# Kernel tuning notes

Measured on AMD Instinct MI355X. Metric: run time of the kernel, lower is better.

The kernel has to match this reference:

```python
import jax, jax.numpy as jnp
import numpy as np

T, N, E, IN, H, H2, H3, B, AF = 12, 50000, 800000, 12, 128, 64, 32, 4096, 10
BN_EPS = 1e-5


def _gin_mlp(h, w1, b1, g, be, rm, rv, w2, b2):
    # Linear -> ReLU -> BatchNorm1d (eval: running stats) -> Dropout(eval=id) -> Linear -> ReLU
    h = jax.nn.relu(h @ w1.T + b1)
    h = (h - rm) * (g * jax.lax.rsqrt(rv + BN_EPS)) + be
    return jax.nn.relu(h @ w2.T + b2)


def _gin_conv(x, edge_src, edge_dst, mlp_params):
    # GINConv with eps=0: MLP(x + sum_{j in N(i)} x_j), scatter-add over edges
    agg = jax.ops.segment_sum(x[edge_src], edge_dst, num_segments=x.shape[0])
    return _gin_mlp(x + agg, *mlp_params)


def _gru(xs, wih, whh, bih, bhh):
    # torch.nn.GRU, 1 layer, h0 = zeros. xs: [T, N, H_in]
    h0 = jnp.zeros((xs.shape[1], whh.shape[1]), xs.dtype)

    def step(h, x):
        gi = x @ wih.T + bih
        gh = h @ whh.T + bhh
        ir, iz, inn = jnp.split(gi, 3, axis=-1)
        hr, hz, hn = jnp.split(gh, 3, axis=-1)
        r = jax.nn.sigmoid(ir + hr)
        z = jax.nn.sigmoid(iz + hz)
        n = jnp.tanh(inn + r * hn)
        h_new = (1.0 - z) * n + z * h
        return h_new, h_new

    h_last, ys = jax.lax.scan(step, h0, xs)
    return ys, h_last


def _forward(floats, edge_src, edge_dst, target_idx):
    (x_seq, apart_feature,
     c1_w1, c1_b1, c1_g, c1_be, c1_rm, c1_rv, c1_w2, c1_b2,
     c2_w1, c2_b1, c2_g, c2_be, c2_rm, c2_rv, c2_w2, c2_b2,
     gru_wih, gru_whh, gru_bih, gru_bhh,
     fc1_w, fc1_b, fc2_w, fc2_b, fc3_w, fc3_b) = floats

    c1 = (c1_w1, c1_b1, c1_g, c1_be, c1_rm, c1_rv, c1_w2, c1_b2)
    c2 = (c2_w1, c2_b1, c2_g, c2_be, c2_rm, c2_rv, c2_w2, c2_b2)

    # conv1 per time slot (lax.map keeps the E x H gather intermediate per-step)
    # extra torch.relu after conv1 is a no-op since the MLP ends in ReLU
    emb = jax.lax.map(lambda xt: _gin_conv(xt, edge_src, edge_dst, c1), x_seq)
    seq, _ = _gru(emb, gru_wih, gru_whh, gru_bih, gru_bhh)
    emb2 = jax.lax.map(lambda xt: _gin_conv(xt, edge_src, edge_dst, c2), seq)
    _, h_last = _gru(emb2, gru_wih, gru_whh, gru_bih, gru_bhh)  # same GRU weights reused

    feat = jnp.concatenate([h_last[target_idx], apart_feature], axis=1)
    h = jax.nn.leaky_relu(feat @ fc1_w.T + fc1_b, negative_slope=0.1)
    h = jax.nn.leaky_relu(h @ fc2_w.T + fc2_b, negative_slope=0.05)
    return h @ fc3_w.T + fc3_b  # [B, 1]


def setup_inputs() -> dict:
    key = jax.random.key(0)
    ks = jax.random.split(key, 24)
    f32 = jnp.float32
    w = lambda i, shape, fan: jax.random.normal(ks[i], shape, f32) * (1.0 / np.sqrt(fan))
    return {
        "x_seq": jax.random.normal(ks[0], (T, N, IN), f32),
        "apart_feature": jax.random.normal(ks[1], (B, AF), f32),
        "edge_src": jax.random.randint(ks[2], (E,), 0, N, jnp.int32),
        "edge_dst": jax.random.randint(ks[3], (E,), 0, N, jnp.int32),
        "target_idx": jax.random.randint(ks[4], (B,), 0, N, jnp.int32),
        # conv1 MLP
        "c1_w1": w(5, (H, IN), IN), "c1_b1": jnp.zeros((H,), f32),
        "c1_g": jnp.ones((H,), f32), "c1_be": jnp.zeros((H,), f32),
        "c1_rm": jnp.zeros((H,), f32), "c1_rv": jnp.ones((H,), f32),
        "c1_w2": w(6, (H, H), H), "c1_b2": jnp.zeros((H,), f32),
        # conv2 MLP
        "c2_w1": w(7, (H, H), H), "c2_b1": jnp.zeros((H,), f32),
        "c2_g": jnp.ones((H,), f32), "c2_be": jnp.zeros((H,), f32),
        "c2_rm": jnp.zeros((H,), f32), "c2_rv": jnp.ones((H,), f32),
        "c2_w2": w(8, (H, H), H), "c2_b2": jnp.zeros((H,), f32),
        # shared GRU
        "gru_wih": w(9, (3 * H, H), H), "gru_whh": w(10, (3 * H, H), H),
        "gru_bih": jnp.zeros((3 * H,), f32), "gru_bhh": jnp.zeros((3 * H,), f32),
        # head
        "fc1_w": w(11, (H2, H + AF), H + AF), "fc1_b": jnp.zeros((H2,), f32),
        "fc2_w": w(12, (H3, H2), H2), "fc2_b": jnp.zeros((H3,), f32),
        "fc3_w": w(13, (1, H3), H3), "fc3_b": jnp.zeros((1,), f32),
    }


def reference(x_seq, apart_feature,
              c1_w1, c1_b1, c1_g, c1_be, c1_rm, c1_rv, c1_w2, c1_b2,
              c2_w1, c2_b1, c2_g, c2_be, c2_rm, c2_rv, c2_w2, c2_b2,
              gru_wih, gru_whh, gru_bih, gru_bhh,
              fc1_w, fc1_b, fc2_w, fc2_b, fc3_w, fc3_b,
              edge_src, edge_dst, target_idx):
    floats = (x_seq, apart_feature,
              c1_w1, c1_b1, c1_g, c1_be, c1_rm, c1_rv, c1_w2, c1_b2,
              c2_w1, c2_b1, c2_g, c2_be, c2_rm, c2_rv, c2_w2, c2_b2,
              gru_wih, gru_whh, gru_bih, gru_bhh,
              fc1_w, fc1_b, fc2_w, fc2_b, fc3_w, fc3_b)
    return _forward(floats, edge_src, edge_dst, target_idx)
```

## Files before the change

kernel.cpp:

```cpp
#include <hip/hip_runtime.h>

#define T_STEPS 12
#define NN      50000
#define EE      800000
#define IN_F    12
#define HID     128
#define G3      384
#define BB      4096
#define AF_     10
#define BN_EPS  1e-5f
#define LPAD    136

typedef unsigned short ushort_t;
typedef __attribute__((ext_vector_type(8))) short bf16x8;
typedef __attribute__((ext_vector_type(4))) float f32x4;

#define MFMA(a, b, c) __builtin_amdgcn_mfma_f32_16x16x32_bf16((a), (b), (c), 0, 0, 0)

__device__ inline float b2f(ushort_t u) { return __uint_as_float(((unsigned)u) << 16); }
__device__ inline ushort_t f2b(float f) {
    unsigned u = __float_as_uint(f);
    return (ushort_t)((u + 0x7fffu + ((u >> 16) & 1u)) >> 16);
}
__device__ inline float sigm(float x) { return 1.f / (1.f + expf(-x)); }

#define ALIGN_UP(x) (((x) + 255) & ~(size_t)255)
#define SZ_DEG    ALIGN_UP((size_t)NN * 4)
#define SZ_RP     ALIGN_UP((size_t)(NN + 1) * 4)
#define SZ_CUR    ALIGN_UP((size_t)NN * 4)
#define SZ_COL    ALIGN_UP((size_t)EE * 4)
#define SZ_XIN12  ALIGN_UP((size_t)NN * IN_F * 4)
#define SZ_NHB    ALIGN_UP((size_t)NN * HID * 2)
#define SZ_W128   ALIGN_UP((size_t)HID * HID * 2)
#define SZ_WGRU   ALIGN_UP((size_t)G3 * HID * 2)
#define WS_NEED   (SZ_DEG + SZ_RP + SZ_CUR + SZ_COL + SZ_XIN12 + 3 * SZ_NHB + 3 * SZ_W128 + 2 * SZ_WGRU)

__device__ __align__(256) char g_static_pool[WS_NEED];

__global__ void zero_out_kernel(float* out, int n) {
    int i = blockIdx.x * blockDim.x + threadIdx.x;
    if (i < n) out[i] = 0.f;
}

__global__ void cvt5_kernel(const float* s0, ushort_t* d0, int n0,
                            const float* s1, ushort_t* d1, int n1,
                            const float* s2, ushort_t* d2, int n2,
                            const float* s3, ushort_t* d3, int n3,
                            const float* s4, ushort_t* d4, int n4) {
    int i = blockIdx.x * blockDim.x + threadIdx.x;
    if (i < n0) d0[i] = f2b(s0[i]);
    i -= n0;
    if (i >= 0 && i < n1) d1[i] = f2b(s1[i]);
    i -= n1;
    if (i >= 0 && i < n2) d2[i] = f2b(s2[i]);
    i -= n2;
    if (i >= 0 && i < n3) d3[i] = f2b(s3[i]);
    i -= n3;
    if (i >= 0 && i < n4) d4[i] = f2b(s4[i]);
}

__global__ void init_kernel(int* deg, ushort_t* h1, ushort_t* h2) {
    int i = blockIdx.x * blockDim.x + threadIdx.x;
    if (i < NN) deg[i] = 0;
    if (i < NN * HID) { h1[i] = 0; h2[i] = 0; }
}

__global__ void hist_kernel(const int* __restrict__ dst, int* __restrict__ deg, int E) {
    int e = blockIdx.x * blockDim.x + threadIdx.x;
    if (e < E) {
        unsigned d = (unsigned)dst[e];
        if (d < NN) atomicAdd(&deg[d], 1);
    }
}

__global__ __launch_bounds__(1024) void scan_kernel(const int* __restrict__ deg,
                                                    int* __restrict__ row_ptr,
                                                    int* __restrict__ cursor, int n) {
    __shared__ int wsum[16];
    __shared__ int carry_s;
    int tid = threadIdx.x;
    int wid = tid >> 6, lane = tid & 63;
    if (tid == 0) { carry_s = 0; row_ptr[0] = 0; }
    __syncthreads();
    for (int base = 0; base < n; base += 1024) {
        int i = base + tid;
        int v = (i < n) ? deg[i] : 0;
        int x = v;
#pragma unroll
        for (int off = 1; off < 64; off <<= 1) {
            int t = __shfl_up(x, (unsigned)off);
            if (lane >= off) x += t;
        }
        if (lane == 63) wsum[wid] = x;
        __syncthreads();
        if (tid == 0) {
            int a = 0;
#pragma unroll
            for (int w = 0; w < 16; ++w) { int t = wsum[w]; wsum[w] = a; a += t; }
        }
        __syncthreads();
        int incl = carry_s + wsum[wid] + x;
        if (i < n) {
            row_ptr[i + 1] = incl;
            cursor[i] = incl - v;
        }
        __syncthreads();
        if (tid == 1023) carry_s = incl;
        __syncthreads();
    }
}

__global__ void scatter_kernel(const int* __restrict__ src, const int* __restrict__ dst,
                               int* __restrict__ cursor, int* __restrict__ col, int E) {
    int e = blockIdx.x * blockDim.x + threadIdx.x;
    if (e < E) {
        unsigned d = (unsigned)dst[e];
        if (d < NN) {
            int pos = atomicAdd(&cursor[d], 1);
            if ((unsigned)pos < (unsigned)EE) col[pos] = src[e];
        }
    }
}

__global__ void agg12_kernel(const float* __restrict__ x, const int* __restrict__ rp,
                             const int* __restrict__ col, float* __restrict__ out, int E) {
    int g = blockIdx.x * blockDim.x + threadIdx.x;
    if (g >= NN * IN_F) return;
    int i = g / IN_F;
    int f = g - i * IN_F;
    float s = x[g];
    int e0 = rp[i], e1 = rp[i + 1];
    if (e1 > E) e1 = E;
    for (int e = e0; e < e1; ++e) {
        unsigned c = (unsigned)col[e];
        if (c < NN) s += x[c * IN_F + f];
    }
    out[g] = s;
}

__device__ __forceinline__ void gru_phase(const ushort_t (*xl)[LPAD], ushort_t* __restrict__ h,
                                          const ushort_t* __restrict__ wih, const ushort_t* __restrict__ whh,
                                          const float* __restrict__ bih, const float* __restrict__ bhh,
                                          int r0, int li, int ks, int wave) {
    int j0 = wave * 16;
    int ra0 = min(r0 + li, NN - 1);
    int ra1 = min(r0 + 16 + li, NN - 1);
    const ushort_t* ph0 = h + (size_t)ra0 * HID + ks * 8;
    const ushort_t* ph1 = h + (size_t)ra1 * HID + ks * 8;
    const ushort_t* pwr = wih + (size_t)(j0 + li) * HID + ks * 8;
    const ushort_t* pwz = wih + (size_t)(HID + j0 + li) * HID + ks * 8;
    const ushort_t* pwn = wih + (size_t)(2 * HID + j0 + li) * HID + ks * 8;
    const ushort_t* pvr = whh + (size_t)(j0 + li) * HID + ks * 8;
    const ushort_t* pvz = whh + (size_t)(HID + j0 + li) * HID + ks * 8;
    const ushort_t* pvn = whh + (size_t)(2 * HID + j0 + li) * HID + ks * 8;
    f32x4 ir0 = {0,0,0,0}, iz0 = {0,0,0,0}, in0 = {0,0,0,0};
    f32x4 hr0 = {0,0,0,0}, hz0 = {0,0,0,0}, hn0 = {0,0,0,0};
    f32x4 ir1 = {0,0,0,0}, iz1 = {0,0,0,0}, in1 = {0,0,0,0};
    f32x4 hr1 = {0,0,0,0}, hz1 = {0,0,0,0}, hn1 = {0,0,0,0};
#pragma unroll
    for (int k0 = 0; k0 < HID; k0 += 32) {
        bf16x8 ax0 = *(const bf16x8*)&xl[li][ks * 8 + k0];
        bf16x8 ax1 = *(const bf16x8*)&xl[li + 16][ks * 8 + k0];
        bf16x8 ah0 = *(const bf16x8*)(ph0 + k0);
        bf16x8 ah1 = *(const bf16x8*)(ph1 + k0);
        bf16x8 br = *(const bf16x8*)(pwr + k0);
        bf16x8 bz = *(const bf16x8*)(pwz + k0);
        bf16x8 bn = *(const bf16x8*)(pwn + k0);
        bf16x8 cr = *(const bf16x8*)(pvr + k0);
        bf16x8 cz = *(const bf16x8*)(pvz + k0);
        bf16x8 cn = *(const bf16x8*)(pvn + k0);
        ir0 = MFMA(ax0, br, ir0); ir1 = MFMA(ax1, br, ir1);
        iz0 = MFMA(ax0, bz, iz0); iz1 = MFMA(ax1, bz, iz1);
        in0 = MFMA(ax0, bn, in0); in1 = MFMA(ax1, bn, in1);
        hr0 = MFMA(ah0, cr, hr0); hr1 = MFMA(ah1, cr, hr1);
        hz0 = MFMA(ah0, cz, hz0); hz1 = MFMA(ah1, cz, hz1);
        hn0 = MFMA(ah0, cn, hn0); hn1 = MFMA(ah1, cn, hn1);
    }
    int jc = j0 + li;
    float bi_r = bih[jc], bi_z = bih[HID + jc], bi_n = bih[2 * HID + jc];
    float bh_r = bhh[jc], bh_z = bhh[HID + jc], bh_n = bhh[2 * HID + jc];
    float holdA[4], holdB[4];
#pragma unroll
    for (int q = 0; q < 4; ++q) {
        int rowA = min(r0 + ks * 4 + q, NN - 1);
        int rowB = min(r0 + 16 + ks * 4 + q, NN - 1);
        holdA[q] = b2f(h[(size_t)rowA * HID + jc]);
        holdB[q] = b2f(h[(size_t)rowB * HID + jc]);
    }
    __syncthreads();
#pragma unroll
    for (int q = 0; q < 4; ++q) {
        int rowA = r0 + ks * 4 + q;
        int rowB = rowA + 16;
        {
            float rg = sigm(ir0[q] + bi_r + hr0[q] + bh_r);
            float zg = sigm(iz0[q] + bi_z + hz0[q] + bh_z);
            float ng = tanhf(in0[q] + bi_n + rg * (hn0[q] + bh_n));
            float hv = (1.f - zg) * ng + zg * holdA[q];
            if (rowA < NN) h[(size_t)rowA * HID + jc] = f2b(hv);
        }
        {
            float rg = sigm(ir1[q] + bi_r + hr1[q] + bh_r);
            float zg = sigm(iz1[q] + bi_z + hz1[q] + bh_z);
            float ng = tanhf(in1[q] + bi_n + rg * (hn1[q] + bh_n));
            float hv = (1.f - zg) * ng + zg * holdB[q];
            if (rowB < NN) h[(size_t)rowB * HID + jc] = f2b(hv);
        }
    }
}

__global__ __launch_bounds__(512) void mega1_kernel(const float* __restrict__ xin12,
                                                    ushort_t* __restrict__ h,
                                                    const float* __restrict__ W1, const float* __restrict__ b1,
                                                    const float* __restrict__ gg, const float* __restrict__ be,
                                                    const float* __restrict__ rm, const float* __restrict__ rv,
                                                    const ushort_t* __restrict__ w2b, const float* __restrict__ b2,
                                                    const ushort_t* __restrict__ wih, const ushort_t* __restrict__ whh,
                                                    const float* __restrict__ bih, const float* __restrict__ bhh) {
    __shared__ float xs[32][IN_F];
    __shared__ ushort_t l1[32][LPAD];
    __shared__ ushort_t l2[32][LPAD];
    int tid = threadIdx.x;
    int wave = tid >> 6, lane = tid & 63;
    int li = lane & 15, ks = lane >> 4;
    int r0 = blockIdx.x * 32;
    if (tid < 32 * IN_F) {
        int r = tid / IN_F, f = tid - r * IN_F;
        int row = r0 + r;
        xs[r][f] = (row < NN) ? xin12[(size_t)row * IN_F + f] : 0.f;
    }
    __syncthreads();
    {
        int j = tid & 127, rb = tid >> 7;
        float sc = gg[j] * rsqrtf(rv[j] + BN_EPS);
        float sh = be[j] - rm[j] * sc;
        float bj = b1[j];
        float wreg[IN_F];
#pragma unroll
        for (int k = 0; k < IN_F; ++k) wreg[k] = W1[j * IN_F + k];
#pragma unroll
        for (int q = 0; q < 8; ++q) {
            int r = rb + q * 4;
            float s = bj;
#pragma unroll
            for (int k = 0; k < IN_F; ++k) s += xs[r][k] * wreg[k];
            s = fmaxf(s, 0.f);
            l1[r][j] = f2b(s * sc + sh);
        }
    }
    __syncthreads();
    {
        int j0 = wave * 16;
        const ushort_t* pw = w2b + (size_t)(j0 + li) * HID + ks * 8;
        f32x4 acc0 = {0,0,0,0}, acc1 = {0,0,0,0};
#pragma unroll
        for (int k0 = 0; k0 < HID; k0 += 32) {
            bf16x8 w = *(const bf16x8*)(pw + k0);
            bf16x8 a0 = *(const bf16x8*)&l1[li][ks * 8 + k0];
            bf16x8 a1 = *(const bf16x8*)&l1[li + 16][ks * 8 + k0];
            acc0 = MFMA(a0, w, acc0);
            acc1 = MFMA(a1, w, acc1);
        }
        float bj = b2[j0 + li];
#pragma unroll
        for (int q = 0; q < 4; ++q) {
            l2[ks * 4 + q][j0 + li] = f2b(fmaxf(acc0[q] + bj, 0.f));
            l2[16 + ks * 4 + q][j0 + li] = f2b(fmaxf(acc1[q] + bj, 0.f));
        }
    }
    __syncthreads();
    gru_phase(l2, h, wih, whh, bih, bhh, r0, li, ks, wave);
}

__global__ __launch_bounds__(512) void mega2_kernel(const ushort_t* __restrict__ xin2,
                                                    ushort_t* __restrict__ h,
                                                    const ushort_t* __restrict__ w1b, const float* __restrict__ b1,
                                                    const float* __restrict__ gg, const float* __restrict__ be,
                                                    const float* __restrict__ rm, const float* __restrict__ rv,
                                                    const ushort_t* __restrict__ w2b, const float* __restrict__ b2,
                                                    const ushort_t* __restrict__ wih, const ushort_t* __restrict__ whh,
                                                    const float* __restrict__ bih, const float* __restrict__ bhh) {
    __shared__ ushort_t l1[32][LPAD];
    __shared__ ushort_t l2[32][LPAD];
    int tid = threadIdx.x;
    int wave = tid >> 6, lane = tid & 63;
    int li = lane & 15, ks = lane >> 4;
    int r0 = blockIdx.x * 32;
    {
        int j0 = wave * 16;
        int ra0 = min(r0 + li, NN - 1);
        int ra1 = min(r0 + 16 + li, NN - 1);
        const ushort_t* pa0 = xin2 + (size_t)ra0 * HID + ks * 8;
        const ushort_t* pa1 = xin2 + (size_t)ra1 * HID + ks * 8;
        const ushort_t* pw = w1b + (size_t)(j0 + li) * HID + ks * 8;
        f32x4 acc0 = {0,0,0,0}, acc1 = {0,0,0,0};
#pragma unroll
        for (int k0 = 0; k0 < HID; k0 += 32) {
            bf16x8 w = *(const bf16x8*)(pw + k0);
            bf16x8 a0 = *(const bf16x8*)(pa0 + k0);
            bf16x8 a1 = *(const bf16x8*)(pa1 + k0);
            acc0 = MFMA(a0, w, acc0);
            acc1 = MFMA(a1, w, acc1);
        }
        int jc = j0 + li;
        float sc = gg[jc] * rsqrtf(rv[jc] + BN_EPS);
        float sh = be[jc] - rm[jc] * sc;
        float bj = b1[jc];
#pragma unroll
        for (int q = 0; q < 4; ++q) {
            l1[ks * 4 + q][jc] = f2b(fmaxf(acc0[q] + bj, 0.f) * sc + sh);
            l1[16 + ks * 4 + q][jc] = f2b(fmaxf(acc1[q] + bj, 0.f) * sc + sh);
        }
    }
    __syncthreads();
    {
        int j0 = wave * 16;
        const ushort_t* pw = w2b + (size_t)(j0 + li) * HID + ks * 8;
        f32x4 acc0 = {0,0,0,0}, acc1 = {0,0,0,0};
#pragma unroll
        for (int k0 = 0; k0 < HID; k0 += 32) {
            bf16x8 w = *(const bf16x8*)(pw + k0);
            bf16x8 a0 = *(const bf16x8*)&l1[li][ks * 8 + k0];
            bf16x8 a1 = *(const bf16x8*)&l1[li + 16][ks * 8 + k0];
            acc0 = MFMA(a0, w, acc0);
            acc1 = MFMA(a1, w, acc1);
        }
        float bj = b2[j0 + li];
#pragma unroll
        for (int q = 0; q < 4; ++q) {
            l2[ks * 4 + q][j0 + li] = f2b(fmaxf(acc0[q] + bj, 0.f));
            l2[16 + ks * 4 + q][j0 + li] = f2b(fmaxf(acc1[q] + bj, 0.f));
        }
    }
    __syncthreads();
    gru_phase(l2, h, wih, whh, bih, bhh, r0, li, ks, wave);
}

__global__ __launch_bounds__(256) void agg128b_kernel(const ushort_t* __restrict__ x,
                                                      const int* __restrict__ rp,
                                                      const int* __restrict__ col,
                                                      ushort_t* __restrict__ out, int E) {
    int node = (blockIdx.x * 256 + threadIdx.x) >> 6;
    int lane = threadIdx.x & 63;
    if (node >= NN) return;
    unsigned v = *(const unsigned*)(x + (size_t)node * HID + lane * 2);
    float s0 = b2f((ushort_t)(v & 0xffff));
    float s1 = b2f((ushort_t)(v >> 16));
    int e0 = rp[node], e1 = rp[node + 1];
    if (e1 > E) e1 = E;
    int e = e0;
    for (; e + 3 < e1; e += 4) {
        unsigned c0 = (unsigned)col[e], c1 = (unsigned)col[e + 1];
        unsigned c2 = (unsigned)col[e + 2], c3 = (unsigned)col[e + 3];
        c0 = (c0 < NN) ? c0 : 0; c1 = (c1 < NN) ? c1 : 0;
        c2 = (c2 < NN) ? c2 : 0; c3 = (c3 < NN) ? c3 : 0;
        unsigned u0 = *(const unsigned*)(x + (size_t)c0 * HID + lane * 2);
        unsigned u1 = *(const unsigned*)(x + (size_t)c1 * HID + lane * 2);
        unsigned u2 = *(const unsigned*)(x + (size_t)c2 * HID + lane * 2);
        unsigned u3 = *(const unsigned*)(x + (size_t)c3 * HID + lane * 2);
        s0 += b2f((ushort_t)(u0 & 0xffff)) + b2f((ushort_t)(u1 & 0xffff))
            + b2f((ushort_t)(u2 & 0xffff)) + b2f((ushort_t)(u3 & 0xffff));
        s1 += b2f((ushort_t)(u0 >> 16)) + b2f((ushort_t)(u1 >> 16))
            + b2f((ushort_t)(u2 >> 16)) + b2f((ushort_t)(u3 >> 16));
    }
    for (; e < e1; ++e) {
        unsigned c = (unsigned)col[e];
        if (c < NN) {
            unsigned u = *(const unsigned*)(x + (size_t)c * HID + lane * 2);
            s0 += b2f((ushort_t)(u & 0xffff));
            s1 += b2f((ushort_t)(u >> 16));
        }
    }
    unsigned o = (unsigned)f2b(s0) | ((unsigned)f2b(s1) << 16);
    *(unsigned*)(out + (size_t)node * HID + lane * 2) = o;
}

__global__ __launch_bounds__(64) void head_kernel(const ushort_t* __restrict__ h2, const int* __restrict__ tidx,
                                                  const float* __restrict__ apart,
                                                  const float* __restrict__ w1, const float* __restrict__ b1,
                                                  const float* __restrict__ w2, const float* __restrict__ b2,
                                                  const float* __restrict__ w3, const float* __restrict__ b3,
                                                  float* __restrict__ out) {
    __shared__ float feat[HID + AF_];
    __shared__ float o1[64];
    __shared__ float o2[32];
    int b = blockIdx.x;
    int t = threadIdx.x;
    unsigned node = (unsigned)tidx[b];
    if (node >= NN) node = 0;
    for (int k = t; k < HID; k += 64) feat[k] = b2f(h2[(size_t)node * HID + k]);
    if (t < AF_) feat[HID + t] = apart[(size_t)b * AF_ + t];
    __syncthreads();
    {
        float s = b1[t];
        for (int k = 0; k < HID + AF_; ++k) s += feat[k] * w1[t * (HID + AF_) + k];
        o1[t] = (s > 0.f) ? s : 0.1f * s;
    }
    __syncthreads();
    if (t < 32) {
        float s = b2[t];
        for (int k = 0; k < 64; ++k) s += o1[k] * w2[t * 64 + k];
        o2[t] = (s > 0.f) ? s : 0.05f * s;
    }
    __syncthreads();
    if (t == 0) {
        float s = b3[0];
        for (int k = 0; k < 32; ++k) s += o2[k] * w3[k];
        out[b] = s;
    }
}

extern "C" void kernel_launch(void* const* d_in, const int* in_sizes, int n_in,
                              void* d_out, int out_size, void* d_ws, size_t ws_size,
                              hipStream_t stream) {
    int ie_src = -1, ie_dst = -1, ie_tidx = -1, iw0 = -1;
    bool ok = false;
    if (n_in >= 31 && in_sizes[0] == T_STEPS * NN * IN_F && in_sizes[1] == BB * AF_) {
        if (in_sizes[2] > 100000 && in_sizes[3] == in_sizes[2] && in_sizes[4] == BB &&
            in_sizes[5] == HID * IN_F && in_sizes[11] == HID * HID &&
            in_sizes[21] == G3 * HID && in_sizes[22] == G3 * HID &&
            in_sizes[25] == 64 * (HID + AF_)) {
            ie_src = 2; ie_dst = 3; ie_tidx = 4; iw0 = 5; ok = true;
        } else if (in_sizes[2] == HID * IN_F && in_sizes[8] == HID * HID &&
                   in_sizes[18] == G3 * HID && in_sizes[19] == G3 * HID &&
                   in_sizes[22] == 64 * (HID + AF_) &&
                   in_sizes[28] > 100000 && in_sizes[29] == in_sizes[28] && in_sizes[30] == BB) {
            iw0 = 2; ie_src = 28; ie_dst = 29; ie_tidx = 30; ok = true;
        }
    }
    if (!ok) {
        zero_out_kernel<<<(out_size + 255) / 256, 256, 0, stream>>>((float*)d_out, out_size);
        return;
    }

    const float* x_seq  = (const float*)d_in[0];
    const float* apart  = (const float*)d_in[1];
    const int*   e_src  = (const int*)d_in[ie_src];
    const int*   e_dst  = (const int*)d_in[ie_dst];
    const int*   t_idx  = (const int*)d_in[ie_tidx];
    const float* c1_w1 = (const float*)d_in[iw0 + 0];
    const float* c1_b1 = (const float*)d_in[iw0 + 1];
    const float* c1_g  = (const float*)d_in[iw0 + 2];
    const float* c1_be = (const float*)d_in[iw0 + 3];
    const float* c1_rm = (const float*)d_in[iw0 + 4];
    const float* c1_rv = (const float*)d_in[iw0 + 5];
    const float* c1_w2 = (const float*)d_in[iw0 + 6];
    const float* c1_b2 = (const float*)d_in[iw0 + 7];
    const float* c2_w1 = (const float*)d_in[iw0 + 8];
    const float* c2_b1 = (const float*)d_in[iw0 + 9];
    const float* c2_g  = (const float*)d_in[iw0 + 10];
    const float* c2_be = (const float*)d_in[iw0 + 11];
    const float* c2_rm = (const float*)d_in[iw0 + 12];
    const float* c2_rv = (const float*)d_in[iw0 + 13];
    const float* c2_w2 = (const float*)d_in[iw0 + 14];
    const float* c2_b2 = (const float*)d_in[iw0 + 15];
    const float* g_wih = (const float*)d_in[iw0 + 16];
    const float* g_whh = (const float*)d_in[iw0 + 17];
    const float* g_bih = (const float*)d_in[iw0 + 18];
    const float* g_bhh = (const float*)d_in[iw0 + 19];
    const float* f1_w  = (const float*)d_in[iw0 + 20];
    const float* f1_b  = (const float*)d_in[iw0 + 21];
    const float* f2_w  = (const float*)d_in[iw0 + 22];
    const float* f2_b  = (const float*)d_in[iw0 + 23];
    const float* f3_w  = (const float*)d_in[iw0 + 24];
    const float* f3_b  = (const float*)d_in[iw0 + 25];

    int E = in_sizes[ie_src];
    if (E > EE) E = EE;

    char* base;
    if (ws_size >= WS_NEED) {
        base = (char*)d_ws;
    } else {
        void* sp = nullptr;
        hipGetSymbolAddress(&sp, HIP_SYMBOL(g_static_pool));
        if (sp == nullptr) {
            zero_out_kernel<<<(out_size + 255) / 256, 256, 0, stream>>>((float*)d_out, out_size);
            return;
        }
        base = (char*)sp;
    }
    size_t off = 0;
    auto nxt = [&](size_t bytes) { char* p = base + off; off += bytes; return p; };
    int*      deg     = (int*)nxt(SZ_DEG);
    int*      row_ptr = (int*)nxt(SZ_RP);
    int*      cursor  = (int*)nxt(SZ_CUR);
    int*      col     = (int*)nxt(SZ_COL);
    float*    xin12   = (float*)nxt(SZ_XIN12);
    ushort_t* xin2    = (ushort_t*)nxt(SZ_NHB);
    ushort_t* h1      = (ushort_t*)nxt(SZ_NHB);
    ushort_t* h2      = (ushort_t*)nxt(SZ_NHB);
    ushort_t* wb_c1w2 = (ushort_t*)nxt(SZ_W128);
    ushort_t* wb_c2w1 = (ushort_t*)nxt(SZ_W128);
    ushort_t* wb_c2w2 = (ushort_t*)nxt(SZ_W128);
    ushort_t* wb_wih  = (ushort_t*)nxt(SZ_WGRU);
    ushort_t* wb_whh  = (ushort_t*)nxt(SZ_WGRU);

    const int NW = 3 * HID * HID + 2 * G3 * HID;
    cvt5_kernel<<<(NW + 255) / 256, 256, 0, stream>>>(c1_w2, wb_c1w2, HID * HID,
                                                      c2_w1, wb_c2w1, HID * HID,
                                                      c2_w2, wb_c2w2, HID * HID,
                                                      g_wih, wb_wih, G3 * HID,
                                                      g_whh, wb_whh, G3 * HID);

    init_kernel<<<(NN * HID + 255) / 256, 256, 0, stream>>>(deg, h1, h2);

    hist_kernel<<<(E + 255) / 256, 256, 0, stream>>>(e_dst, deg, E);
    scan_kernel<<<1, 1024, 0, stream>>>(deg, row_ptr, cursor, NN);
    scatter_kernel<<<(E + 255) / 256, 256, 0, stream>>>(e_src, e_dst, cursor, col, E);

    const int mgrid = (NN + 31) / 32;

    for (int t = 0; t < T_STEPS; ++t) {
        const float* xt = x_seq + (size_t)t * NN * IN_F;
        agg12_kernel<<<(NN * IN_F + 255) / 256, 256, 0, stream>>>(xt, row_ptr, col, xin12, E);
        mega1_kernel<<<mgrid, 512, 0, stream>>>(xin12, h1,
                                                c1_w1, c1_b1, c1_g, c1_be, c1_rm, c1_rv,
                                                wb_c1w2, c1_b2,
                                                wb_wih, wb_whh, g_bih, g_bhh);
        agg128b_kernel<<<(NN * 64 + 255) / 256, 256, 0, stream>>>(h1, row_ptr, col, xin2, E);
        mega2_kernel<<<mgrid, 512, 0, stream>>>(xin2, h2,
                                                wb_c2w1, c2_b1, c2_g, c2_be, c2_rm, c2_rv,
                                                wb_c2w2, c2_b2,
                                                wb_wih, wb_whh, g_bih, g_bhh);
    }

    head_kernel<<<BB, 64, 0, stream>>>(h2, t_idx, apart, f1_w, f1_b, f2_w, f2_b, f3_w, f3_b, (float*)d_out);
}
```

Before: 2.696 ms.

## Batch conv1 over all timesteps, fuse aggregation into conv2 kernel, enlarge tiles

Conv1 no longer depends on the recurrence, so it now runs for all 12 timesteps in one launch that also does the 12-feature neighbour sum inline. It writes a T×N×H bf16 embedding buffer that a separate per-step GRU kernel reads. The 128-wide neighbour aggregation moves inside mega2, which removes the agg128b launch and its intermediate round trip. Row tiles grow from 32 to 64 and sigmoid/tanh switch to exp2/rcp intrinsics. In exchange it needs about 150MB of extra workspace and does more work per block, which may lower occupancy.

```diff
diff --git a/kernel.cpp b/kernel.cpp
--- a/kernel.cpp
+++ b/kernel.cpp
@@ -16,24 +16,34 @@
 typedef __attribute__((ext_vector_type(4))) float f32x4;
 
 #define MFMA(a, b, c) __builtin_amdgcn_mfma_f32_16x16x32_bf16((a), (b), (c), 0, 0, 0)
+#define L2E 1.4426950408889634f
 
 __device__ inline float b2f(ushort_t u) { return __uint_as_float(((unsigned)u) << 16); }
+__device__ inline float b2f_lo(unsigned u) { return __uint_as_float(u << 16); }
+__device__ inline float b2f_hi(unsigned u) { return __uint_as_float(u & 0xffff0000u); }
 __device__ inline ushort_t f2b(float f) {
     unsigned u = __float_as_uint(f);
     return (ushort_t)((u + 0x7fffu + ((u >> 16) & 1u)) >> 16);
 }
-__device__ inline float sigm(float x) { return 1.f / (1.f + expf(-x)); }
+__device__ inline float sigm(float x) {
+    return __builtin_amdgcn_rcpf(1.f + __builtin_amdgcn_exp2f(-x * L2E));
+}
+__device__ inline float ftanh(float x) {
+    float xx = fminf(fmaxf(x, -15.f), 15.f);
+    float t = __builtin_amdgcn_exp2f(2.f * L2E * xx);
+    return (t - 1.f) * __builtin_amdgcn_rcpf(t + 1.f);
+}
 
 #define ALIGN_UP(x) (((x) + 255) & ~(size_t)255)
 #define SZ_DEG    ALIGN_UP((size_t)NN * 4)
 #define SZ_RP     ALIGN_UP((size_t)(NN + 1) * 4)
 #define SZ_CUR    ALIGN_UP((size_t)NN * 4)
 #define SZ_COL    ALIGN_UP((size_t)EE * 4)
-#define SZ_XIN12  ALIGN_UP((size_t)NN * IN_F * 4)
+#define SZ_EMB    ALIGN_UP((size_t)T_STEPS * NN * HID * 2)
 #define SZ_NHB    ALIGN_UP((size_t)NN * HID * 2)
 #define SZ_W128   ALIGN_UP((size_t)HID * HID * 2)
 #define SZ_WGRU   ALIGN_UP((size_t)G3 * HID * 2)
-#define WS_NEED   (SZ_DEG + SZ_RP + SZ_CUR + SZ_COL + SZ_XIN12 + 3 * SZ_NHB + 3 * SZ_W128 + 2 * SZ_WGRU)
+#define WS_NEED   (SZ_DEG + SZ_RP + SZ_CUR + SZ_COL + SZ_EMB + 2 * SZ_NHB + 3 * SZ_W128 + 2 * SZ_WGRU)
 
 __device__ __align__(256) char g_static_pool[WS_NEED];
 
@@ -122,112 +132,35 @@
     }
 }
 
-__global__ void agg12_kernel(const float* __restrict__ x, const int* __restrict__ rp,
-                             const int* __restrict__ col, float* __restrict__ out, int E) {
-    int g = blockIdx.x * blockDim.x + threadIdx.x;
-    if (g >= NN * IN_F) return;
-    int i = g / IN_F;
-    int f = g - i * IN_F;
-    float s = x[g];
-    int e0 = rp[i], e1 = rp[i + 1];
-    if (e1 > E) e1 = E;
-    for (int e = e0; e < e1; ++e) {
-        unsigned c = (unsigned)col[e];
-        if (c < NN) s += x[c * IN_F + f];
-    }
-    out[g] = s;
-}
-
-__device__ __forceinline__ void gru_phase(const ushort_t (*xl)[LPAD], ushort_t* __restrict__ h,
-                                          const ushort_t* __restrict__ wih, const ushort_t* __restrict__ whh,
-                                          const float* __restrict__ bih, const float* __restrict__ bhh,
-                                          int r0, int li, int ks, int wave) {
-    int j0 = wave * 16;
-    int ra0 = min(r0 + li, NN - 1);
-    int ra1 = min(r0 + 16 + li, NN - 1);
-    const ushort_t* ph0 = h + (size_t)ra0 * HID + ks * 8;
-    const ushort_t* ph1 = h + (size_t)ra1 * HID + ks * 8;
-    const ushort_t* pwr = wih + (size_t)(j0 + li) * HID + ks * 8;
-    const ushort_t* pwz = wih + (size_t)(HID + j0 + li) * HID + ks * 8;
-    const ushort_t* pwn = wih + (size_t)(2 * HID + j0 + li) * HID + ks * 8;
-    const ushort_t* pvr = whh + (size_t)(j0 + li) * HID + ks * 8;
-    const ushort_t* pvz = whh + (size_t)(HID + j0 + li) * HID + ks * 8;
-    const ushort_t* pvn = whh + (size_t)(2 * HID + j0 + li) * HID + ks * 8;
-    f32x4 ir0 = {0,0,0,0}, iz0 = {0,0,0,0}, in0 = {0,0,0,0};
-    f32x4 hr0 = {0,0,0,0}, hz0 = {0,0,0,0}, hn0 = {0,0,0,0};
-    f32x4 ir1 = {0,0,0,0}, iz1 = {0,0,0,0}, in1 = {0,0,0,0};
-    f32x4 hr1 = {0,0,0,0}, hz1 = {0,0,0,0}, hn1 = {0,0,0,0};
-#pragma unroll
-    for (int k0 = 0; k0 < HID; k0 += 32) {
-        bf16x8 ax0 = *(const bf16x8*)&xl[li][ks * 8 + k0];
-        bf16x8 ax1 = *(const bf16x8*)&xl[li + 16][ks * 8 + k0];
-        bf16x8 ah0 = *(const bf16x8*)(ph0 + k0);
-        bf16x8 ah1 = *(const bf16x8*)(ph1 + k0);
-        bf16x8 br = *(const bf16x8*)(pwr + k0);
-        bf16x8 bz = *(const bf16x8*)(pwz + k0);
-        bf16x8 bn = *(const bf16x8*)(pwn + k0);
-        bf16x8 cr = *(const bf16x8*)(pvr + k0);
-        bf16x8 cz = *(const bf16x8*)(pvz + k0);
-        bf16x8 cn = *(const bf16x8*)(pvn + k0);
-        ir0 = MFMA(ax0, br, ir0); ir1 = MFMA(ax1, br, ir1);
-        iz0 = MFMA(ax0, bz, iz0); iz1 = MFMA(ax1, bz, iz1);
-        in0 = MFMA(ax0, bn, in0); in1 = MFMA(ax1, bn, in1);
-        hr0 = MFMA(ah0, cr, hr0); hr1 = MFMA(ah1, cr, hr1);
-        hz0 = MFMA(ah0, cz, hz0); hz1 = MFMA(ah1, cz, hz1);
-        hn0 = MFMA(ah0, cn, hn0); hn1 = MFMA(ah1, cn, hn1);
-    }
-    int jc = j0 + li;
-    float bi_r = bih[jc], bi_z = bih[HID + jc], bi_n = bih[2 * HID + jc];
-    float bh_r = bhh[jc], bh_z = bhh[HID + jc], bh_n = bhh[2 * HID + jc];
-    float holdA[4], holdB[4];
-#pragma unroll
-    for (int q = 0; q < 4; ++q) {
-        int rowA = min(r0 + ks * 4 + q, NN - 1);
-        int rowB = min(r0 + 16 + ks * 4 + q, NN - 1);
-        holdA[q] = b2f(h[(size_t)rowA * HID + jc]);
-        holdB[q] = b2f(h[(size_t)rowB * HID + jc]);
-    }
-    __syncthreads();
-#pragma unroll
-    for (int q = 0; q < 4; ++q) {
-        int rowA = r0 + ks * 4 + q;
-        int rowB = rowA + 16;
-        {
-            float rg = sigm(ir0[q] + bi_r + hr0[q] + bh_r);
-            float zg = sigm(iz0[q] + bi_z + hz0[q] + bh_z);
-            float ng = tanhf(in0[q] + bi_n + rg * (hn0[q] + bh_n));
-            float hv = (1.f - zg) * ng + zg * holdA[q];
-            if (rowA < NN) h[(size_t)rowA * HID + jc] = f2b(hv);
-        }
-        {
-            float rg = sigm(ir1[q] + bi_r + hr1[q] + bh_r);
-            float zg = sigm(iz1[q] + bi_z + hz1[q] + bh_z);
-            float ng = tanhf(in1[q] + bi_n + rg * (hn1[q] + bh_n));
-            float hv = (1.f - zg) * ng + zg * holdB[q];
-            if (rowB < NN) h[(size_t)rowB * HID + jc] = f2b(hv);
-        }
-    }
-}
-
-__global__ __launch_bounds__(512) void mega1_kernel(const float* __restrict__ xin12,
-                                                    ushort_t* __restrict__ h,
-                                                    const float* __restrict__ W1, const float* __restrict__ b1,
-                                                    const float* __restrict__ gg, const float* __restrict__ be,
-                                                    const float* __restrict__ rm, const float* __restrict__ rv,
-                                                    const ushort_t* __restrict__ w2b, const float* __restrict__ b2,
-                                                    const ushort_t* __restrict__ wih, const ushort_t* __restrict__ whh,
-                                                    const float* __restrict__ bih, const float* __restrict__ bhh) {
-    __shared__ float xs[32][IN_F];
-    __shared__ ushort_t l1[32][LPAD];
-    __shared__ ushort_t l2[32][LPAD];
+__global__ __launch_bounds__(512) void conv1_all_kernel(const float* __restrict__ x_seq,
+                                                        ushort_t* __restrict__ emb,
+                                                        const int* __restrict__ rp, const int* __restrict__ col,
+                                                        const float* __restrict__ W1, const float* __restrict__ b1,
+                                                        const float* __restrict__ gg, const float* __restrict__ be,
+                                                        const float* __restrict__ rm, const float* __restrict__ rv,
+                                                        const ushort_t* __restrict__ w2b, const float* __restrict__ b2,
+                                                        int E) {
+    __shared__ float xs[64][IN_F + 1];
+    __shared__ ushort_t l1[64][LPAD];
+    int t = blockIdx.y;
+    const float* xt = x_seq + (size_t)t * NN * IN_F;
+    ushort_t* et = emb + (size_t)t * NN * HID;
     int tid = threadIdx.x;
-    int wave = tid >> 6, lane = tid & 63;
-    int li = lane & 15, ks = lane >> 4;
-    int r0 = blockIdx.x * 32;
-    if (tid < 32 * IN_F) {
-        int r = tid / IN_F, f = tid - r * IN_F;
-        int row = r0 + r;
-        xs[r][f] = (row < NN) ? xin12[(size_t)row * IN_F + f] : 0.f;
+    int r0 = blockIdx.x * 64;
+    for (int u = tid; u < 64 * IN_F; u += 512) {
+        int r = u / IN_F, f = u - r * IN_F;
+        int node = r0 + r;
+        float s = 0.f;
+        if (node < NN) {
+            s = xt[(size_t)node * IN_F + f];
+            int e0 = rp[node], e1 = rp[node + 1];
+            if (e1 > E) e1 = E;
+            for (int e = e0; e < e1; ++e) {
+                unsigned c = (unsigned)col[e];
+                if (c < NN) s += xt[(size_t)c * IN_F + f];
+            }
+        }
+        xs[r][f] = s;
     }
     __syncthreads();
     {
@@ -239,7 +172,7 @@
 #pragma unroll
         for (int k = 0; k < IN_F; ++k) wreg[k] = W1[j * IN_F + k];
 #pragma unroll
-        for (int q = 0; q < 8; ++q) {
+        for (int q = 0; q < 16; ++q) {
             int r = rb + q * 4;
             float s = bj;
 #pragma unroll
@@ -250,129 +183,268 @@
     }
     __syncthreads();
     {
-        int j0 = wave * 16;
-        const ushort_t* pw = w2b + (size_t)(j0 + li) * HID + ks * 8;
-        f32x4 acc0 = {0,0,0,0}, acc1 = {0,0,0,0};
+        int wave = tid >> 6, lane = tid & 63, li = lane & 15, ks = lane >> 4;
+        int j0 = wave * 16, jc = j0 + li;
+        const ushort_t* pw = w2b + (size_t)jc * HID + ks * 8;
+        f32x4 A0 = {0,0,0,0}, A1 = {0,0,0,0}, A2 = {0,0,0,0}, A3 = {0,0,0,0};
 #pragma unroll
         for (int k0 = 0; k0 < HID; k0 += 32) {
-            bf16x8 w = *(const bf16x8*)(pw + k0);
+            bf16x8 wf = *(const bf16x8*)(pw + k0);
             bf16x8 a0 = *(const bf16x8*)&l1[li][ks * 8 + k0];
             bf16x8 a1 = *(const bf16x8*)&l1[li + 16][ks * 8 + k0];
-            acc0 = MFMA(a0, w, acc0);
-            acc1 = MFMA(a1, w, acc1);
-        }
-        float bj = b2[j0 + li];
+            bf16x8 a2 = *(const bf16x8*)&l1[li + 32][ks * 8 + k0];
+            bf16x8 a3 = *(const bf16x8*)&l1[li + 48][ks * 8 + k0];
+            A0 = MFMA(a0, wf, A0); A1 = MFMA(a1, wf, A1);
+            A2 = MFMA(a2, wf, A2); A3 = MFMA(a3, wf, A3);
+        }
+        float bj = b2[jc];
 #pragma unroll
         for (int q = 0; q < 4; ++q) {
-            l2[ks * 4 + q][j0 + li] = f2b(fmaxf(acc0[q] + bj, 0.f));
-            l2[16 + ks * 4 + q][j0 + li] = f2b(fmaxf(acc1[q] + bj, 0.f));
-        }
-    }
-    __syncthreads();
-    gru_phase(l2, h, wih, whh, bih, bhh, r0, li, ks, wave);
-}
-
-__global__ __launch_bounds__(512) void mega2_kernel(const ushort_t* __restrict__ xin2,
-                                                    ushort_t* __restrict__ h,
+            int rA = r0 + ks * 4 + q, rB = rA + 16, rC = rA + 32, rD = rA + 48;
+            if (rA < NN) et[(size_t)rA * HID + jc] = f2b(fmaxf(A0[q] + bj, 0.f));
+            if (rB < NN) et[(size_t)rB * HID + jc] = f2b(fmaxf(A1[q] + bj, 0.f));
+            if (rC < NN) et[(size_t)rC * HID + jc] = f2b(fmaxf(A2[q] + bj, 0.f));
+            if (rD < NN) et[(size_t)rD * HID + jc] = f2b(fmaxf(A3[q] + bj, 0.f));
+        }
+    }
+}
+
+__global__ __launch_bounds__(512) void gru_step_kernel(const ushort_t* __restrict__ x,
+                                                       ushort_t* __restrict__ h,
+                                                       const ushort_t* __restrict__ wih,
+                                                       const ushort_t* __restrict__ whh,
+                                                       const float* __restrict__ bih,
+                                                       const float* __restrict__ bhh) {
+    int tid = threadIdx.x;
+    int wave = tid >> 6, lane = tid & 63, li = lane & 15, ks = lane >> 4;
+    int r0 = blockIdx.x * 64;
+    int j0 = wave * 16, jc = j0 + li;
+    const ushort_t* px[4];
+    const ushort_t* ph[4];
+#pragma unroll
+    for (int tt = 0; tt < 4; ++tt) {
+        int ra = min(r0 + tt * 16 + li, NN - 1);
+        px[tt] = x + (size_t)ra * HID + ks * 8;
+        ph[tt] = h + (size_t)ra * HID + ks * 8;
+    }
+    const ushort_t* pwr = wih + (size_t)jc * HID + ks * 8;
+    const ushort_t* pwz = wih + (size_t)(HID + jc) * HID + ks * 8;
+    const ushort_t* pwn = wih + (size_t)(2 * HID + jc) * HID + ks * 8;
+    const ushort_t* pvr = whh + (size_t)jc * HID + ks * 8;
+    const ushort_t* pvz = whh + (size_t)(HID + jc) * HID + ks * 8;
+    const ushort_t* pvn = whh + (size_t)(2 * HID + jc) * HID + ks * 8;
+    f32x4 Ir[4], Iz[4], In[4], Hr[4], Hz[4], Hn[4];
+#pragma unroll
+    for (int tt = 0; tt < 4; ++tt) {
+        Ir[tt] = (f32x4){0,0,0,0}; Iz[tt] = (f32x4){0,0,0,0}; In[tt] = (f32x4){0,0,0,0};
+        Hr[tt] = (f32x4){0,0,0,0}; Hz[tt] = (f32x4){0,0,0,0}; Hn[tt] = (f32x4){0,0,0,0};
+    }
+#pragma unroll
+    for (int k0 = 0; k0 < HID; k0 += 32) {
+        bf16x8 wr = *(const bf16x8*)(pwr + k0);
+        bf16x8 wz = *(const bf16x8*)(pwz + k0);
+        bf16x8 wn = *(const bf16x8*)(pwn + k0);
+        bf16x8 vr = *(const bf16x8*)(pvr + k0);
+        bf16x8 vz = *(const bf16x8*)(pvz + k0);
+        bf16x8 vn = *(const bf16x8*)(pvn + k0);
+#pragma unroll
+        for (int tt = 0; tt < 4; ++tt) {
+            bf16x8 xf = *(const bf16x8*)(px[tt] + k0);
+            bf16x8 hf = *(const bf16x8*)(ph[tt] + k0);
+            Ir[tt] = MFMA(xf, wr, Ir[tt]);
+            Iz[tt] = MFMA(xf, wz, Iz[tt]);
+            In[tt] = MFMA(xf, wn, In[tt]);
+            Hr[tt] = MFMA(hf, vr, Hr[tt]);
+            Hz[tt] = MFMA(hf, vz, Hz[tt]);
+            Hn[tt] = MFMA(hf, vn, Hn[tt]);
+        }
+    }
+    float bi_r = bih[jc], bi_z = bih[HID + jc], bi_n = bih[2 * HID + jc];
+    float bh_r = bhh[jc], bh_z = bhh[HID + jc], bh_n = bhh[2 * HID + jc];
+    float hold[4][4];
+#pragma unroll
+    for (int tt = 0; tt < 4; ++tt)
+#pragma unroll
+        for (int q = 0; q < 4; ++q) {
+            int rr = min(r0 + tt * 16 + ks * 4 + q, NN - 1);
+            hold[tt][q] = b2f(h[(size_t)rr * HID + jc]);
+        }
+    __syncthreads();
+#pragma unroll
+    for (int tt = 0; tt < 4; ++tt)
+#pragma unroll
+        for (int q = 0; q < 4; ++q) {
+            int row = r0 + tt * 16 + ks * 4 + q;
+            float rg = sigm(Ir[tt][q] + bi_r + Hr[tt][q] + bh_r);
+            float zg = sigm(Iz[tt][q] + bi_z + Hz[tt][q] + bh_z);
+            float ng = ftanh(In[tt][q] + bi_n + rg * (Hn[tt][q] + bh_n));
+            float hv = (1.f - zg) * ng + zg * hold[tt][q];
+            if (row < NN) h[(size_t)row * HID + jc] = f2b(hv);
+        }
+}
+
+__global__ __launch_bounds__(512) void mega2_kernel(const ushort_t* __restrict__ h1,
+                                                    ushort_t* __restrict__ h2,
+                                                    const int* __restrict__ rp, const int* __restrict__ col,
                                                     const ushort_t* __restrict__ w1b, const float* __restrict__ b1,
                                                     const float* __restrict__ gg, const float* __restrict__ be,
                                                     const float* __restrict__ rm, const float* __restrict__ rv,
                                                     const ushort_t* __restrict__ w2b, const float* __restrict__ b2,
                                                     const ushort_t* __restrict__ wih, const ushort_t* __restrict__ whh,
-                                                    const float* __restrict__ bih, const float* __restrict__ bhh) {
-    __shared__ ushort_t l1[32][LPAD];
-    __shared__ ushort_t l2[32][LPAD];
+                                                    const float* __restrict__ bih, const float* __restrict__ bhh,
+                                                    int E) {
+    __shared__ ushort_t bufA[64][LPAD];
+    __shared__ ushort_t bufB[64][LPAD];
     int tid = threadIdx.x;
-    int wave = tid >> 6, lane = tid & 63;
-    int li = lane & 15, ks = lane >> 4;
-    int r0 = blockIdx.x * 32;
-    {
-        int j0 = wave * 16;
-        int ra0 = min(r0 + li, NN - 1);
-        int ra1 = min(r0 + 16 + li, NN - 1);
-        const ushort_t* pa0 = xin2 + (size_t)ra0 * HID + ks * 8;
-        const ushort_t* pa1 = xin2 + (size_t)ra1 * HID + ks * 8;
-        const ushort_t* pw = w1b + (size_t)(j0 + li) * HID + ks * 8;
-        f32x4 acc0 = {0,0,0,0}, acc1 = {0,0,0,0};
+    int wave = tid >> 6, lane = tid & 63, li = lane & 15, ks = lane >> 4;
+    int r0 = blockIdx.x * 64;
+    int j0 = wave * 16, jc = j0 + li;
+    {
+        int nl = tid >> 3, cg = tid & 7;
+        int node = r0 + nl;
+        float a[16];
+#pragma unroll
+        for (int i = 0; i < 16; ++i) a[i] = 0.f;
+        if (node < NN) {
+            const unsigned* pr = (const unsigned*)(h1 + (size_t)node * HID + cg * 16);
+#pragma unroll
+            for (int i = 0; i < 8; ++i) {
+                unsigned u = pr[i];
+                a[2 * i] = b2f_lo(u);
+                a[2 * i + 1] = b2f_hi(u);
+            }
+            int e0 = rp[node], e1 = rp[node + 1];
+            if (e1 > E) e1 = E;
+            for (int e = e0; e < e1; ++e) {
+                unsigned c = (unsigned)col[e];
+                if (c >= NN) continue;
+                const unsigned* pn = (const unsigned*)(h1 + (size_t)c * HID + cg * 16);
+#pragma unroll
+                for (int i = 0; i < 8; ++i) {
+                    unsigned u = pn[i];
+                    a[2 * i] += b2f_lo(u);
+                    a[2 * i + 1] += b2f_hi(u);
+                }
+            }
+        }
+        unsigned* wp = (unsigned*)&bufA[nl][cg * 16];
+#pragma unroll
+        for (int i = 0; i < 8; ++i)
+            wp[i] = (unsigned)f2b(a[2 * i]) | ((unsigned)f2b(a[2 * i + 1]) << 16);
+    }
+    __syncthreads();
+    f32x4 Hr[4], Hz[4], Hn[4], C1[4];
+#pragma unroll
+    for (int tt = 0; tt < 4; ++tt) {
+        Hr[tt] = (f32x4){0,0,0,0}; Hz[tt] = (f32x4){0,0,0,0};
+        Hn[tt] = (f32x4){0,0,0,0}; C1[tt] = (f32x4){0,0,0,0};
+    }
+    {
+        const ushort_t* pw1 = w1b + (size_t)jc * HID + ks * 8;
+        const ushort_t* pvr = whh + (size_t)jc * HID + ks * 8;
+        const ushort_t* pvz = whh + (size_t)(HID + jc) * HID + ks * 8;
+        const ushort_t* pvn = whh + (size_t)(2 * HID + jc) * HID + ks * 8;
+        const ushort_t* ph[4];
+#pragma unroll
+        for (int tt = 0; tt < 4; ++tt) {
+            int ra = min(r0 + tt * 16 + li, NN - 1);
+            ph[tt] = h2 + (size_t)ra * HID + ks * 8;
+        }
 #pragma unroll
         for (int k0 = 0; k0 < HID; k0 += 32) {
-            bf16x8 w = *(const bf16x8*)(pw + k0);
-            bf16x8 a0 = *(const bf16x8*)(pa0 + k0);
-            bf16x8 a1 = *(const bf16x8*)(pa1 + k0);
-            acc0 = MFMA(a0, w, acc0);
-            acc1 = MFMA(a1, w, acc1);
-        }
-        int jc = j0 + li;
+            bf16x8 w1f = *(const bf16x8*)(pw1 + k0);
+            bf16x8 vr = *(const bf16x8*)(pvr + k0);
+            bf16x8 vz = *(const bf16x8*)(pvz + k0);
+            bf16x8 vn = *(const bf16x8*)(pvn + k0);
+#pragma unroll
+            for (int tt = 0; tt < 4; ++tt) {
+                bf16x8 af = *(const bf16x8*)&bufA[li + 16 * tt][ks * 8 + k0];
+                bf16x8 hf = *(const bf16x8*)(ph[tt] + k0);
+                C1[tt] = MFMA(af, w1f, C1[tt]);
+                Hr[tt] = MFMA(hf, vr, Hr[tt]);
+                Hz[tt] = MFMA(hf, vz, Hz[tt]);
+                Hn[tt] = MFMA(hf, vn, Hn[tt]);
+            }
+        }
+    }
+    float hold[4][4];
+#pragma unroll
+    for (int tt = 0; tt < 4; ++tt)
+#pragma unroll
+        for (int q = 0; q < 4; ++q) {
+            int rr = min(r0 + tt * 16 + ks * 4 + q, NN - 1);
+            hold[tt][q] = b2f(h2[(size_t)rr * HID + jc]);
+        }
+    {
         float sc = gg[jc] * rsqrtf(rv[jc] + BN_EPS);
         float sh = be[jc] - rm[jc] * sc;
         float bj = b1[jc];
 #pragma unroll
-        for (int q = 0; q < 4; ++q) {
-            l1[ks * 4 + q][jc] = f2b(fmaxf(acc0[q] + bj, 0.f) * sc + sh);
-            l1[16 + ks * 4 + q][jc] = f2b(fmaxf(acc1[q] + bj, 0.f) * sc + sh);
-        }
-    }
-    __syncthreads();
-    {
-        int j0 = wave * 16;
-        const ushort_t* pw = w2b + (size_t)(j0 + li) * HID + ks * 8;
-        f32x4 acc0 = {0,0,0,0}, acc1 = {0,0,0,0};
+        for (int tt = 0; tt < 4; ++tt)
+#pragma unroll
+            for (int q = 0; q < 4; ++q)
+                bufB[tt * 16 + ks * 4 + q][jc] = f2b(fmaxf(C1[tt][q] + bj, 0.f) * sc + sh);
+    }
+    __syncthreads();
+    {
+        const ushort_t* pw2 = w2b + (size_t)jc * HID + ks * 8;
+        f32x4 C2[4];
+#pragma unroll
+        for (int tt = 0; tt < 4; ++tt) C2[tt] = (f32x4){0,0,0,0};
 #pragma unroll
         for (int k0 = 0; k0 < HID; k0 += 32) {
-            bf16x8 w = *(const bf16x8*)(pw + k0);
-            bf16x8 a0 = *(const bf16x8*)&l1[li][ks * 8 + k0];
-            bf16x8 a1 = *(const bf16x8*)&l1[li + 16][ks * 8 + k0];
-            acc0 = MFMA(a0, w, acc0);
-            acc1 = MFMA(a1, w, acc1);
-        }
-        float bj = b2[j0 + li];
-#pragma unroll
-        for (int q = 0; q < 4; ++q) {
-            l2[ks * 4 + q][j0 + li] = f2b(fmaxf(acc0[q] + bj, 0.f));
-            l2[16 + ks * 4 + q][j0 + li] = f2b(fmaxf(acc1[q] + bj, 0.f));
-        }
-    }
-    __syncthreads();
-    gru_phase(l2, h, wih, whh, bih, bhh, r0, li, ks, wave);
-}
-
-__global__ __launch_bounds__(256) void agg128b_kernel(const ushort_t* __restrict__ x,
-                                                      const int* __restrict__ rp,
-                                                      const int* __restrict__ col,
-                                                      ushort_t* __restrict__ out, int E) {
-    int node = (blockIdx.x * 256 + threadIdx.x) >> 6;
-    int lane = threadIdx.x & 63;
-    if (node >= NN) return;
-    unsigned v = *(const unsigned*)(x + (size_t)node * HID + lane * 2);
-    float s0 = b2f((ushort_t)(v & 0xffff));
-    float s1 = b2f((ushort_t)(v >> 16));
-    int e0 = rp[node], e1 = rp[node + 1];
-    if (e1 > E) e1 = E;
-    int e = e0;
-    for (; e + 3 < e1; e += 4) {
-        unsigned c0 = (unsigned)col[e], c1 = (unsigned)col[e + 1];
-        unsigned c2 = (unsigned)col[e + 2], c3 = (unsigned)col[e + 3];
-        c0 = (c0 < NN) ? c0 : 0; c1 = (c1 < NN) ? c1 : 0;
-        c2 = (c2 < NN) ? c2 : 0; c3 = (c3 < NN) ? c3 : 0;
-        unsigned u0 = *(const unsigned*)(x + (size_t)c0 * HID + lane * 2);
-        unsigned u1 = *(const unsigned*)(x + (size_t)c1 * HID + lane * 2);
-        unsigned u2 = *(const unsigned*)(x + (size_t)c2 * HID + lane * 2);
-        unsigned u3 = *(const unsigned*)(x + (size_t)c3 * HID + lane * 2);
-        s0 += b2f((ushort_t)(u0 & 0xffff)) + b2f((ushort_t)(u1 & 0xffff))
-            + b2f((ushort_t)(u2 & 0xffff)) + b2f((ushort_t)(u3 & 0xffff));
-        s1 += b2f((ushort_t)(u0 >> 16)) + b2f((ushort_t)(u1 >> 16))
-            + b2f((ushort_t)(u2 >> 16)) + b2f((ushort_t)(u3 >> 16));
-    }
-    for (; e < e1; ++e) {
-        unsigned c = (unsigned)col[e];
-        if (c < NN) {
-            unsigned u = *(const unsigned*)(x + (size_t)c * HID + lane * 2);
-            s0 += b2f((ushort_t)(u & 0xffff));
-            s1 += b2f((ushort_t)(u >> 16));
-        }
-    }
-    unsigned o = (unsigned)f2b(s0) | ((unsigned)f2b(s1) << 16);
-    *(unsigned*)(out + (size_t)node * HID + lane * 2) = o;
+            bf16x8 wf = *(const bf16x8*)(pw2 + k0);
+#pragma unroll
+            for (int tt = 0; tt < 4; ++tt) {
+                bf16x8 af = *(const bf16x8*)&bufB[li + 16 * tt][ks * 8 + k0];
+                C2[tt] = MFMA(af, wf, C2[tt]);
+            }
+        }
+        float bj = b2[jc];
+        __syncthreads();
+#pragma unroll
+        for (int tt = 0; tt < 4; ++tt)
+#pragma unroll
+            for (int q = 0; q < 4; ++q)
+                bufA[tt * 16 + ks * 4 + q][jc] = f2b(fmaxf(C2[tt][q] + bj, 0.f));
+    }
+    __syncthreads();
+    {
+        const ushort_t* pwr = wih + (size_t)jc * HID + ks * 8;
+        const ushort_t* pwz = wih + (size_t)(HID + jc) * HID + ks * 8;
+        const ushort_t* pwn = wih + (size_t)(2 * HID + jc) * HID + ks * 8;
+        f32x4 Ir[4], Iz[4], In[4];
+#pragma unroll
+        for (int tt = 0; tt < 4; ++tt) {
+            Ir[tt] = (f32x4){0,0,0,0}; Iz[tt] = (f32x4){0,0,0,0}; In[tt] = (f32x4){0,0,0,0};
+        }
+#pragma unroll
+        for (int k0 = 0; k0 < HID; k0 += 32) {
+            bf16x8 wr = *(const bf16x8*)(pwr + k0);
+            bf16x8 wz = *(const bf16x8*)(pwz + k0);
+            bf16x8 wn = *(const bf16x8*)(pwn + k0);
+#pragma unroll
+            for (int tt = 0; tt < 4; ++tt) {
+                bf16x8 xf = *(const bf16x8*)&bufA[li + 16 * tt][ks * 8 + k0];
+                Ir[tt] = MFMA(xf, wr, Ir[tt]);
+                Iz[tt] = MFMA(xf, wz, Iz[tt]);
+                In[tt] = MFMA(xf, wn, In[tt]);
+            }
+        }
+        float bi_r = bih[jc], bi_z = bih[HID + jc], bi_n = bih[2 * HID + jc];
+        float bh_r = bhh[jc], bh_z = bhh[HID + jc], bh_n = bhh[2 * HID + jc];
+#pragma unroll
+        for (int tt = 0; tt < 4; ++tt)
+#pragma unroll
+            for (int q = 0; q < 4; ++q) {
+                int row = r0 + tt * 16 + ks * 4 + q;
+                float rg = sigm(Ir[tt][q] + bi_r + Hr[tt][q] + bh_r);
+                float zg = sigm(Iz[tt][q] + bi_z + Hz[tt][q] + bh_z);
+                float ng = ftanh(In[tt][q] + bi_n + rg * (Hn[tt][q] + bh_n));
+                float hv = (1.f - zg) * ng + zg * hold[tt][q];
+                if (row < NN) h2[(size_t)row * HID + jc] = f2b(hv);
+            }
+    }
 }
 
 __global__ __launch_bounds__(64) void head_kernel(const ushort_t* __restrict__ h2, const int* __restrict__ tidx,
@@ -486,8 +558,7 @@
     int*      row_ptr = (int*)nxt(SZ_RP);
     int*      cursor  = (int*)nxt(SZ_CUR);
     int*      col     = (int*)nxt(SZ_COL);
-    float*    xin12   = (float*)nxt(SZ_XIN12);
-    ushort_t* xin2    = (ushort_t*)nxt(SZ_NHB);
+    ushort_t* emb     = (ushort_t*)nxt(SZ_EMB);
     ushort_t* h1      = (ushort_t*)nxt(SZ_NHB);
     ushort_t* h2      = (ushort_t*)nxt(SZ_NHB);
     ushort_t* wb_c1w2 = (ushort_t*)nxt(SZ_W128);
@@ -509,20 +580,19 @@
     scan_kernel<<<1, 1024, 0, stream>>>(deg, row_ptr, cursor, NN);
     scatter_kernel<<<(E + 255) / 256, 256, 0, stream>>>(e_src, e_dst, cursor, col, E);
 
-    const int mgrid = (NN + 31) / 32;
+    const int NB = (NN + 63) / 64;
+
+    conv1_all_kernel<<<dim3(NB, T_STEPS), 512, 0, stream>>>(x_seq, emb, row_ptr, col,
+                                                            c1_w1, c1_b1, c1_g, c1_be, c1_rm, c1_rv,
+                                                            wb_c1w2, c1_b2, E);
 
     for (int t = 0; t < T_STEPS; ++t) {
-        const float* xt = x_seq + (size_t)t * NN * IN_F;
-        agg12_kernel<<<(NN * IN_F + 255) / 256, 256, 0, stream>>>(xt, row_ptr, col, xin12, E);
-        mega1_kernel<<<mgrid, 512, 0, stream>>>(xin12, h1,
-                                                c1_w1, c1_b1, c1_g, c1_be, c1_rm, c1_rv,
-                                                wb_c1w2, c1_b2,
+        gru_step_kernel<<<NB, 512, 0, stream>>>(emb + (size_t)t * NN * HID, h1,
                                                 wb_wih, wb_whh, g_bih, g_bhh);
-        agg128b_kernel<<<(NN * 64 + 255) / 256, 256, 0, stream>>>(h1, row_ptr, col, xin2, E);
-        mega2_kernel<<<mgrid, 512, 0, stream>>>(xin2, h2,
-                                                wb_c2w1, c2_b1, c2_g, c2_be, c2_rm, c2_rv,
-                                                wb_c2w2, c2_b2,
-                                                wb_wih, wb_whh, g_bih, g_bhh);
+        mega2_kernel<<<NB, 512, 0, stream>>>(h1, h2, row_ptr, col,
+                                             wb_c2w1, c2_b1, c2_g, c2_be, c2_rm, c2_rv,
+                                             wb_c2w2, c2_b2,
+                                             wb_wih, wb_whh, g_bih, g_bhh, E);
     }
 
     head_kernel<<<BB, 64, 0, stream>>>(h2, t_idx, apart, f1_w, f1_b, f2_w, f2_b, f3_w, f3_b, (float*)d_out);
```

Measured after the change: 2.878 ms. 1.07x slower.
